# Kernel tuning notes

Hardware: AMD Instinct MI355X
Metric: run time of the kernel (lower is better)

## Reference

```python
import jax, jax.numpy as jnp
import numpy as np

IN_FEAT = 78
C = 128          # out_channels
H = 8            # nheads (layer 1)
B = 1024         # num graphs / batch
NPG = 32         # nodes per graph
N = B * NPG      # total nodes
EPG = 128        # edges per graph
E = B * EPG
GENE = 18000
PROT = 6688
FP = 2048        # drr/drc fingerprint size
N_TASKS = 1


def _lin(key, fan_in, fan_out):
    kw, kb = jax.random.split(key)
    s = 1.0 / np.sqrt(fan_in)
    W = jax.random.uniform(kw, (fan_in, fan_out), jnp.float32, -s, s)
    b = jax.random.uniform(kb, (fan_out,), jnp.float32, -s, s)
    return W, b


def setup_inputs() -> dict:
    key = jax.random.key(0)
    ks = jax.random.split(key, 32)
    goff = jnp.repeat(jnp.arange(B, dtype=jnp.int64) * NPG, EPG)
    e1s = jax.random.randint(ks[0], (E,), 0, NPG, dtype=jnp.int64) + goff
    e1d = jax.random.randint(ks[1], (E,), 0, NPG, dtype=jnp.int64) + goff
    e2s = jax.random.randint(ks[2], (E,), 0, NPG, dtype=jnp.int64) + goff
    e2d = jax.random.randint(ks[3], (E,), 0, NPG, dtype=jnp.int64) + goff
    inp = {
        "x1": jax.random.normal(ks[4], (N, IN_FEAT), jnp.float32),
        "x2": jax.random.normal(ks[5], (N, IN_FEAT), jnp.float32),
        "gene_exp": jax.random.uniform(ks[6], (B, GENE), jnp.float32),
        "drr": jax.random.uniform(ks[7], (B, FP), jnp.float32),
        "drc": jax.random.uniform(ks[8], (B, FP), jnp.float32),
        "prot_exp": jax.random.normal(ks[9], (B, PROT), jnp.float32),
        "edge_index1": jnp.stack([e1s, e1d]),
        "edge_index2": jnp.stack([e2s, e2d]),
        "batch": jnp.repeat(jnp.arange(B, dtype=jnp.int64), NPG),
    }
    W1, b1 = _lin(ks[10], IN_FEAT, H * C)
    inp.update(W_gat1=W1, b_gat1=b1,
               a_src1=jax.random.normal(ks[11], (H, C), jnp.float32) * 0.1,
               a_dst1=jax.random.normal(ks[12], (H, C), jnp.float32) * 0.1)
    # GAT layer 2: 1024 -> 128, 1 head
    W2, b2 = _lin(ks[13], H * C, C)
    inp.update(W_gat2=W2, b_gat2=b2,
               a_src2=jax.random.normal(ks[14], (1, C), jnp.float32) * 0.1,
               a_dst2=jax.random.normal(ks[15], (1, C), jnp.float32) * 0.1)
    inp["W_fcg"], inp["b_fcg"] = _lin(ks[16], C, C)
    # reduction MLP: gene -> 2048 -> 512 -> 2C
    inp["Wr1"], inp["br1"] = _lin(ks[17], GENE, 2048)
    inp["Wr2"], inp["br2"] = _lin(ks[18], 2048, 512)
    inp["Wr3"], inp["br3"] = _lin(ks[19], 512, 2 * C)
    # prot MLP: 6688 -> 1024 -> 512 -> 2C
    inp["Wp1"], inp["bp1"] = _lin(ks[20], PROT, 1024)
    inp["Wp2"], inp["bp2"] = _lin(ks[21], 1024, 512)
    inp["Wp3"], inp["bp3"] = _lin(ks[22], 512, 2 * C)
    # fingerprint fusion linears
    inp["Wdrr"], inp["bdrr"] = _lin(ks[23], C + FP, C + FP)
    inp["Wdrc"], inp["bdrc"] = _lin(ks[24], C + FP, C + FP)
    # predictor (3 layers): in = 2*(C+FP) + 2C + 2C = 4864 -> 512 -> 256 -> n_tasks
    in_dim = 2 * (C + FP) + 2 * C + 2 * C
    inp["Wf1"], inp["bf1"] = _lin(ks[25], in_dim, 512)
    inp["Wf2"], inp["bf2"] = _lin(ks[26], 512, 256)
    inp["Wout"], inp["bout"] = _lin(ks[27], 256, N_TASKS)
    return inp


def _gat(x, src, dst, W, a_src, a_dst, b, heads, ch):
    n = x.shape[0]
    # add self-loops (PyG GATConv default)
    sl = jnp.arange(n, dtype=src.dtype)
    src = jnp.concatenate([src, sl])
    dst = jnp.concatenate([dst, sl])
    h = (x @ W).reshape(n, heads, ch)                    # [N,H,C]
    a_s = (h * a_src).sum(-1)                            # [N,H]
    a_d = (h * a_dst).sum(-1)
    e = jax.nn.leaky_relu(a_s[src] + a_d[dst], 0.2)      # [E',H]
    m = jax.ops.segment_max(e, dst, num_segments=n)
    ex = jnp.exp(e - m[dst])
    den = jax.ops.segment_sum(ex, dst, num_segments=n)
    alpha = ex / (den[dst] + 1e-16)
    out = jax.ops.segment_sum(h[src] * alpha[:, :, None], dst, num_segments=n)
    return out.reshape(n, heads * ch) + b


def reference(x1, x2, gene_exp, drr, drc, prot_exp,
              W_gat1, b_gat1, a_src1, a_dst1,
              W_gat2, b_gat2, a_src2, a_dst2,
              W_fcg, b_fcg,
              Wr1, br1, Wr2, br2, Wr3, br3,
              Wp1, bp1, Wp2, bp2, Wp3, bp3,
              Wdrr, bdrr, Wdrc, bdrc,
              Wf1, bf1, Wf2, bf2, Wout, bout,
              edge_index1, edge_index2, batch):
    nb = gene_exp.shape[0]

    def drug_branch(x, ei):
        x = jax.nn.elu(_gat(x, ei[0], ei[1], W_gat1, a_src1, a_dst1, b_gat1, H, C))
        x = jax.nn.elu(_gat(x, ei[0], ei[1], W_gat2, a_src2, a_dst2, b_gat2, 1, C))
        x = jax.ops.segment_max(x, batch, num_segments=nb)   # global max pool
        return jax.nn.relu(x @ W_fcg + b_fcg)

    g1 = drug_branch(x1, edge_index1)
    g2 = drug_branch(x2, edge_index2)

    # gene branch: L2 row-normalize then MLP (dropout off at inference)
    norm = jnp.sqrt((gene_exp * gene_exp).sum(1, keepdims=True))
    cell = gene_exp / jnp.maximum(norm, 1e-12)
    cell = jax.nn.relu(cell @ Wr1 + br1)
    cell = jax.nn.relu(cell @ Wr2 + br2)
    cell_vec = jax.nn.relu(cell @ Wr3 + br3)

    # protein branch
    p = prot_exp.reshape(-1, PROT)
    p = jax.nn.elu(p @ Wp1 + bp1)
    p = jax.nn.elu(p @ Wp2 + bp2)
    p = jax.nn.relu(p @ Wp3 + bp3)

    # fingerprint fusion
    d1 = jnp.concatenate([g1, drr], axis=1)
    d2 = jnp.concatenate([g2, drc], axis=1)
    d1 = jax.nn.relu(d1 @ Wdrr + bdrr)
    d2 = jax.nn.relu(d2 @ Wdrc + bdrc)

    y = jnp.concatenate([d1, d2, cell_vec, p], axis=1)
    # 3-layer predictor
    y = jax.nn.relu(y @ Wf1 + bf1)
    y = jax.nn.relu(y @ Wf2 + bf2)
    out = y @ Wout + bout
    return out
```

## Files before the change

### kernel.cpp

```cpp
#include <hip/hip_runtime.h>
#include <math.h>

#define BATCH   1024
#define NPG     32
#define NNODES  (BATCH * NPG)
#define EPG     128
#define INFEAT  78
#define CCH     128
#define NHEAD   8
#define GENE    18000
#define GENEP   18016
#define PROT    6688
#define FPD     2048

#define ACT_NONE 0
#define ACT_RELU 1
#define ACT_ELU  2

typedef unsigned short ushort_t;
typedef __bf16 bf16x8_t __attribute__((ext_vector_type(8)));
typedef float  f32x4_t  __attribute__((ext_vector_type(4)));

__device__ __forceinline__ float b2f(ushort_t u) {
    return __uint_as_float(((unsigned)u) << 16);
}
__device__ __forceinline__ ushort_t f2b(float f) {
    unsigned x = __float_as_uint(f);
    return (ushort_t)((x + 0x7fffu + ((x >> 16) & 1u)) >> 16);
}

#define GBM 128
#define GBN 128
#define GBK 32

__device__ __forceinline__ void gemm_core(
    const ushort_t* __restrict__ A, const ushort_t* __restrict__ BT,
    int K, int kb, int ke, int row0, int col0,
    ushort_t* Asl, ushort_t* Bsl, f32x4_t acc[4][4])
{
    const int tid  = threadIdx.x;
    const int wave = tid >> 6;
    const int lane = tid & 63;
    const int wr   = wave >> 1;
    const int wc   = wave & 1;
    const int srow = lane >> 2;
    const int skel = (lane & 3) * 8;

    for (int k0 = kb; k0 < ke; k0 += GBK) {
        __syncthreads();
        #pragma unroll
        for (int t = 0; t < 2; ++t) {
            const int rg = wave * 32 + t * 16;
            const ushort_t* ga = A + (size_t)(row0 + rg + srow) * K + k0 + skel;
            __builtin_amdgcn_global_load_lds(
                (const __attribute__((address_space(1))) void*)ga,
                (__attribute__((address_space(3))) void*)&Asl[rg * GBK], 16, 0, 0);
            const ushort_t* gb = BT + (size_t)(col0 + rg + srow) * K + k0 + skel;
            __builtin_amdgcn_global_load_lds(
                (const __attribute__((address_space(1))) void*)gb,
                (__attribute__((address_space(3))) void*)&Bsl[rg * GBK], 16, 0, 0);
        }
        __syncthreads();

        const int fr = lane & 15;
        const int fq = lane >> 4;
        bf16x8_t av[4], bv[4];
        #pragma unroll
        for (int i = 0; i < 4; ++i)
            av[i] = *(const bf16x8_t*)&Asl[(wr * 64 + i * 16 + fr) * GBK + fq * 8];
        #pragma unroll
        for (int j = 0; j < 4; ++j)
            bv[j] = *(const bf16x8_t*)&Bsl[(wc * 64 + j * 16 + fr) * GBK + fq * 8];
        #pragma unroll
        for (int i = 0; i < 4; ++i)
            #pragma unroll
            for (int j = 0; j < 4; ++j)
                acc[i][j] = __builtin_amdgcn_mfma_f32_16x16x32_bf16(
                    av[i], bv[j], acc[i][j], 0, 0, 0);
    }
}

__global__ __launch_bounds__(256) void gemm_bf16_kernel(
    const ushort_t* __restrict__ A, const ushort_t* __restrict__ BT,
    const float* __restrict__ bias, ushort_t* __restrict__ C,
    int M, int N, int K, int act)
{
    __shared__ ushort_t Asl[GBM * GBK];
    __shared__ ushort_t Bsl[GBN * GBK];
    const int lane = threadIdx.x & 63;
    const int wave = threadIdx.x >> 6;
    const int wr = wave >> 1, wc = wave & 1;
    const int row0 = blockIdx.y * GBM;
    const int col0 = blockIdx.x * GBN;

    f32x4_t acc[4][4] = {};
    gemm_core(A, BT, K, 0, K, row0, col0, Asl, Bsl, acc);

    const int fr = lane & 15;
    const int fq = lane >> 4;
    #pragma unroll
    for (int i = 0; i < 4; ++i) {
        #pragma unroll
        for (int j = 0; j < 4; ++j) {
            const int gn = col0 + wc * 64 + j * 16 + fr;
            const float bb = bias ? bias[gn] : 0.0f;
            #pragma unroll
            for (int r = 0; r < 4; ++r) {
                const int gm = row0 + wr * 64 + i * 16 + fq * 4 + r;
                float v = acc[i][j][r] + bb;
                if (act == ACT_RELU)     v = fmaxf(v, 0.0f);
                else if (act == ACT_ELU) v = (v > 0.0f) ? v : (expf(v) - 1.0f);
                C[(size_t)gm * N + gn] = f2b(v);
            }
        }
    }
}

__global__ __launch_bounds__(256) void gemm_bf16_part_kernel(
    const ushort_t* __restrict__ A, const ushort_t* __restrict__ BT,
    float* __restrict__ part, int M, int N, int K, int KC)
{
    __shared__ ushort_t Asl[GBM * GBK];
    __shared__ ushort_t Bsl[GBN * GBK];
    const int lane = threadIdx.x & 63;
    const int wave = threadIdx.x >> 6;
    const int wr = wave >> 1, wc = wave & 1;
    const int row0 = blockIdx.y * GBM;
    const int col0 = blockIdx.x * GBN;
    const int z    = blockIdx.z;
    const int kb   = z * KC;
    const int ke   = min(K, kb + KC);

    f32x4_t acc[4][4] = {};
    gemm_core(A, BT, K, kb, ke, row0, col0, Asl, Bsl, acc);

    const int fr = lane & 15;
    const int fq = lane >> 4;
    float* po = part + (size_t)z * M * N;
    #pragma unroll
    for (int i = 0; i < 4; ++i)
        #pragma unroll
        for (int j = 0; j < 4; ++j) {
            const int gn = col0 + wc * 64 + j * 16 + fr;
            #pragma unroll
            for (int r = 0; r < 4; ++r) {
                const int gm = row0 + wr * 64 + i * 16 + fq * 4 + r;
                po[(size_t)gm * N + gn] = acc[i][j][r];
            }
        }
}

__global__ __launch_bounds__(256) void reduce_kernel(
    const float* __restrict__ part, const float* __restrict__ bias,
    ushort_t* __restrict__ C, int MN, int N, int S, int act)
{
    int i4 = (blockIdx.x * 256 + threadIdx.x) * 4;
    if (i4 >= MN) return;
    float4 s = *(const float4*)&part[i4];
    for (int z = 1; z < S; ++z) {
        float4 v = *(const float4*)&part[(size_t)z * MN + i4];
        s.x += v.x; s.y += v.y; s.z += v.z; s.w += v.w;
    }
    const int n = i4 % N;
    float o[4] = { s.x, s.y, s.z, s.w };
    if (bias) { o[0] += bias[n]; o[1] += bias[n+1]; o[2] += bias[n+2]; o[3] += bias[n+3]; }
    unsigned pk[2];
    ushort_t r[4];
    #pragma unroll
    for (int k = 0; k < 4; ++k) {
        float v = o[k];
        if (act == ACT_RELU)     v = fmaxf(v, 0.0f);
        else if (act == ACT_ELU) v = (v > 0.0f) ? v : (expf(v) - 1.0f);
        r[k] = f2b(v);
    }
    pk[0] = (unsigned)r[0] | ((unsigned)r[1] << 16);
    pk[1] = (unsigned)r[2] | ((unsigned)r[3] << 16);
    *(uint2*)&C[i4] = make_uint2(pk[0], pk[1]);
}

__global__ __launch_bounds__(256) void cast_rows_kernel(
    const float* __restrict__ src, const float* __restrict__ rowscale,
    ushort_t* __restrict__ dst, int R, int Cin, int Cpad)
{
    int idx = blockIdx.x * 256 + threadIdx.x;
    if (idx >= R * Cpad) return;
    int r = idx / Cpad, c = idx - r * Cpad;
    float v = 0.0f;
    if (c < Cin) {
        v = src[(size_t)r * Cin + c];
        if (rowscale) v *= rowscale[r];
    }
    dst[idx] = f2b(v);
}

__global__ __launch_bounds__(256) void castT_kernel(
    const float* __restrict__ W, ushort_t* __restrict__ WT,
    int K, int N, int Kpad)
{
    __shared__ float t[32][33];
    const int nb = blockIdx.x * 32, kb = blockIdx.y * 32;
    const int x = threadIdx.x & 31, y = threadIdx.x >> 5;
    #pragma unroll
    for (int yy = 0; yy < 32; yy += 8) {
        int k = kb + y + yy, n = nb + x;
        t[y + yy][x] = (k < K && n < N) ? W[(size_t)k * N + n] : 0.0f;
    }
    __syncthreads();
    #pragma unroll
    for (int yy = 0; yy < 32; yy += 8) {
        int n = nb + y + yy, kk = kb + x;
        if (n < N && kk < Kpad) WT[(size_t)n * Kpad + kk] = f2b(t[x][y + yy]);
    }
}

__device__ __forceinline__ unsigned enc_f(float f) {
    unsigned u = __float_as_uint(f);
    return (u >> 31) ? ~u : (u | 0x80000000u);
}
__device__ __forceinline__ float dec_f(unsigned e) {
    return (e >> 31) ? __uint_as_float(e ^ 0x80000000u) : __uint_as_float(~e);
}

template <int POOL>
__global__ __launch_bounds__(256) void gat_fused_kernel(
    const ushort_t* __restrict__ h, const int* __restrict__ esrc,
    const int* __restrict__ edst, const float* __restrict__ a_src,
    const float* __restrict__ a_dst, const float* __restrict__ bias,
    ushort_t* __restrict__ out, int H)
{
    const int g    = blockIdx.x / H;
    const int hd   = blockIdx.x % H;
    const int tid  = threadIdx.x;
    const int lane = tid & 63;
    const int wave = tid >> 6;
    const int base = g * NPG;
    const int HC   = H * CCH;

    __shared__ float h_l[NPG][CCH];
    __shared__ float At[NPG][NPG];
    __shared__ float asv[CCH], adv[CCH];
    __shared__ float as_l[NPG], ad_l[NPG];
    __shared__ unsigned m_l[NPG];
    __shared__ float den_l[NPG];
    __shared__ float sc_l[EPG + NPG];
    __shared__ unsigned char s_l[EPG + NPG], d_l[EPG + NPG];
    __shared__ float ptmp[2][CCH];

    {
        const int r4 = tid >> 6;
        const int cp = (tid & 63) * 2;
        #pragma unroll
        for (int rr = 0; rr < NPG; rr += 4) {
            const int r = rr + r4;
            unsigned v = *(const unsigned*)(h + (size_t)(base + r) * HC + hd * CCH + cp);
            h_l[r][cp]     = b2f((ushort_t)(v & 0xffff));
            h_l[r][cp + 1] = b2f((ushort_t)(v >> 16));
        }
    }
    #pragma unroll
    for (int i = tid; i < NPG * NPG; i += 256) ((float*)At)[i] = 0.0f;
    if (tid < CCH) asv[tid] = a_src[hd * CCH + tid];
    else           adv[tid - CCH] = a_dst[hd * CCH + tid - CCH];
    if (tid < NPG) { m_l[tid] = 0u; den_l[tid] = 0.0f; }
    __syncthreads();

    for (int n = wave; n < NPG; n += 4) {
        float v0 = h_l[n][lane], v1 = h_l[n][lane + 64];
        float s = v0 * asv[lane] + v1 * asv[lane + 64];
        float d = v0 * adv[lane] + v1 * adv[lane + 64];
        #pragma unroll
        for (int o = 32; o > 0; o >>= 1) {
            s += __shfl_xor(s, o, 64);
            d += __shfl_xor(d, o, 64);
        }
        if (lane == 0) { as_l[n] = s; ad_l[n] = d; }
    }
    __syncthreads();

    if (tid < EPG + NPG) {
        int s, d;
        if (tid < EPG) {
            s = esrc[g * EPG + tid] - base;
            d = edst[g * EPG + tid] - base;
        } else {
            s = d = tid - EPG;
        }
        float e = as_l[s] + ad_l[d];
        e = (e >= 0.0f) ? e : 0.2f * e;
        sc_l[tid] = e;
        s_l[tid] = (unsigned char)s;
        d_l[tid] = (unsigned char)d;
        atomicMax(&m_l[d], enc_f(e));
    }
    __syncthreads();

    if (tid < EPG + NPG) {
        float ex = expf(sc_l[tid] - dec_f(m_l[d_l[tid]]));
        sc_l[tid] = ex;
        atomicAdd(&den_l[d_l[tid]], ex);
    }
    __syncthreads();

    if (tid < EPG + NPG) {
        float al = sc_l[tid] / (den_l[d_l[tid]] + 1e-16f);
        atomicAdd(&At[s_l[tid]][d_l[tid]], al);
    }
    __syncthreads();

    const int c    = tid & 127;
    const int half = tid >> 7;
    float acc[16] = {};
    #pragma unroll 4
    for (int s = 0; s < NPG; ++s) {
        const float hv = h_l[s][c];
        const float4* ap = (const float4*)&At[s][half * 16];
        #pragma unroll
        for (int q = 0; q < 4; ++q) {
            float4 av = ap[q];
            acc[q * 4 + 0] += av.x * hv;
            acc[q * 4 + 1] += av.y * hv;
            acc[q * 4 + 2] += av.z * hv;
            acc[q * 4 + 3] += av.w * hv;
        }
    }

    const float bb = bias[hd * CCH + c];
    if (POOL) {
        float m = -INFINITY;
        #pragma unroll
        for (int r = 0; r < 16; ++r) {
            float v = acc[r] + bb;
            v = (v > 0.0f) ? v : (expf(v) - 1.0f);
            m = fmaxf(m, v);
        }
        ptmp[half][c] = m;
        __syncthreads();
        if (tid < CCH)
            out[(size_t)g * CCH + tid] = f2b(fmaxf(ptmp[0][tid], ptmp[1][tid]));
    } else {
        #pragma unroll
        for (int r = 0; r < 16; ++r) {
            float v = acc[r] + bb;
            v = (v > 0.0f) ? v : (expf(v) - 1.0f);
            out[(size_t)(base + half * 16 + r) * HC + hd * CCH + c] = f2b(v);
        }
    }
}

__global__ __launch_bounds__(256) void rownorm_kernel(
    const float* __restrict__ x, float* __restrict__ inv, int K)
{
    const int row = blockIdx.x;
    const int tid = threadIdx.x;
    const float* xp = x + (size_t)row * K;
    float s = 0.f;
    for (int k = tid; k < K; k += 256) { float v = xp[k]; s += v * v; }
    __shared__ float red[256];
    red[tid] = s;
    __syncthreads();
    for (int o = 128; o > 0; o >>= 1) {
        if (tid < o) red[tid] += red[tid + o];
        __syncthreads();
    }
    if (tid == 0) inv[row] = 1.0f / fmaxf(sqrtf(red[0]), 1e-12f);
}

__global__ __launch_bounds__(256) void copyb_kernel(
    ushort_t* __restrict__ dst, int ld, int off,
    const ushort_t* __restrict__ src, int rows, int cols)
{
    int idx = blockIdx.x * 256 + threadIdx.x;
    if (idx >= rows * cols) return;
    int r = idx / cols, c = idx - r * cols;
    dst[(size_t)r * ld + off + c] = src[idx];
}

__global__ __launch_bounds__(256) void castcols_kernel(
    ushort_t* __restrict__ dst, int ld, int off,
    const float* __restrict__ src, int rows, int cols)
{
    int idx = blockIdx.x * 256 + threadIdx.x;
    if (idx >= rows * cols) return;
    int r = idx / cols, c = idx - r * cols;
    dst[(size_t)r * ld + off + c] = f2b(src[idx]);
}

__global__ __launch_bounds__(256) void final_kernel(
    const ushort_t* __restrict__ y, const float* __restrict__ w,
    const float* __restrict__ b, float* __restrict__ out)
{
    const int row = blockIdx.x;
    const int tid = threadIdx.x;
    float v = b2f(y[(size_t)row * 256 + tid]) * w[tid];
    __shared__ float red[256];
    red[tid] = v;
    __syncthreads();
    for (int o = 128; o > 0; o >>= 1) {
        if (tid < o) red[tid] += red[tid + o];
        __syncthreads();
    }
    if (tid == 0) out[row] = red[0] + b[0];
}

static inline void launch_gemm(const ushort_t* A, const ushort_t* BT,
                               const float* bias, ushort_t* C,
                               int M, int N, int K, int act, hipStream_t stream)
{
    dim3 grid(N / GBN, M / GBM);
    gemm_bf16_kernel<<<grid, 256, 0, stream>>>(A, BT, bias, C, M, N, K, act);
}

static inline void launch_gemm_sk(const ushort_t* A, const ushort_t* BT,
                                  const float* bias, ushort_t* C, float* part,
                                  int M, int N, int K, int S, int act,
                                  hipStream_t stream)
{
    if (S <= 1) { launch_gemm(A, BT, bias, C, M, N, K, act, stream); return; }
    const int iters = K / GBK;
    const int ipc   = (iters + S - 1) / S;
    const int S_eff = (iters + ipc - 1) / ipc;
    const int KC    = ipc * GBK;
    dim3 grid(N / GBN, M / GBM, S_eff);
    gemm_bf16_part_kernel<<<grid, 256, 0, stream>>>(A, BT, part, M, N, K, KC);
    const int MN = M * N;
    reduce_kernel<<<(MN / 4 + 255) / 256, 256, 0, stream>>>(
        part, bias, C, MN, N, S_eff, act);
}

static inline void launch_castT(const float* W, ushort_t* WT, int K, int N,
                                int Kpad, hipStream_t stream)
{
    dim3 grid((N + 31) / 32, (Kpad + 31) / 32);
    castT_kernel<<<grid, 256, 0, stream>>>(W, WT, K, N, Kpad);
}

extern "C" void kernel_launch(void* const* d_in, const int* in_sizes, int n_in,
                              void* d_out, int out_size, void* d_ws, size_t ws_size,
                              hipStream_t stream)
{
    const float* x1      = (const float*)d_in[0];
    const float* x2      = (const float*)d_in[1];
    const float* gene    = (const float*)d_in[2];
    const float* drr     = (const float*)d_in[3];
    const float* drc     = (const float*)d_in[4];
    const float* prot    = (const float*)d_in[5];
    const int*   ei1     = (const int*)d_in[6];
    const int*   ei2     = (const int*)d_in[7];
    const float* W_gat1  = (const float*)d_in[9];
    const float* b_gat1  = (const float*)d_in[10];
    const float* a_src1  = (const float*)d_in[11];
    const float* a_dst1  = (const float*)d_in[12];
    const float* W_gat2  = (const float*)d_in[13];
    const float* b_gat2  = (const float*)d_in[14];
    const float* a_src2  = (const float*)d_in[15];
    const float* a_dst2  = (const float*)d_in[16];
    const float* W_fcg   = (const float*)d_in[17];
    const float* b_fcg   = (const float*)d_in[18];
    const float* Wr1     = (const float*)d_in[19];
    const float* br1     = (const float*)d_in[20];
    const float* Wr2     = (const float*)d_in[21];
    const float* br2     = (const float*)d_in[22];
    const float* Wr3     = (const float*)d_in[23];
    const float* br3     = (const float*)d_in[24];
    const float* Wp1     = (const float*)d_in[25];
    const float* bp1     = (const float*)d_in[26];
    const float* Wp2     = (const float*)d_in[27];
    const float* bp2     = (const float*)d_in[28];
    const float* Wp3     = (const float*)d_in[29];
    const float* bp3     = (const float*)d_in[30];
    const float* Wdrr    = (const float*)d_in[31];
    const float* bdrr    = (const float*)d_in[32];
    const float* Wdrc    = (const float*)d_in[33];
    const float* bdrc    = (const float*)d_in[34];
    const float* Wf1     = (const float*)d_in[35];
    const float* bf1     = (const float*)d_in[36];
    const float* Wf2     = (const float*)d_in[37];
    const float* bf2     = (const float*)d_in[38];
    const float* Wout    = (const float*)d_in[39];
    const float* bout    = (const float*)d_in[40];
    float* outp = (float*)d_out;

    char* ws = (char*)d_ws;
    size_t off = 0;
    auto alloc = [&](size_t bytes) -> char* {
        char* r = ws + off;
        off += (bytes + 255) & ~(size_t)255;
        return r;
    };

    char* BIG0 = alloc(134217728);
    char* BIG1 = alloc(67108864);

    ushort_t* go1f   = (ushort_t*)BIG0;
    ushort_t* h1     = (ushort_t*)BIG1;
    float*    part   = (float*)BIG1;
    ushort_t* WT_r1  = (ushort_t*)(BIG0 + 0);
    ushort_t* gene_nb= (ushort_t*)(BIG0 + 73793536);
    ushort_t* cell1  = (ushort_t*)(BIG0 + 110690304);
    ushort_t* WT_r2  = (ushort_t*)(BIG0 + 114884608);
    ushort_t* WT_p2  = (ushort_t*)(BIG0 + 116981760);
    ushort_t* WT_p1  = (ushort_t*)(BIG0 + 118030336);

    ushort_t* xb     = (ushort_t*)alloc((size_t)NNODES * 96 * 2);
    char*     h2reg  = alloc((size_t)2 * NNODES * 128 * 2);
    char*     catreg = alloc((size_t)2 * 1024 * 2176 * 2);
    ushort_t* h2f    = (ushort_t*)h2reg;
    ushort_t* protb  = (ushort_t*)h2reg;
    ushort_t* cat1   = (ushort_t*)catreg;
    ushort_t* cat2   = (ushort_t*)(catreg + (size_t)1024 * 2176 * 2);
    ushort_t* pooled = (ushort_t*)alloc((size_t)2 * BATCH * 128 * 2);
    ushort_t* gpair  = (ushort_t*)alloc((size_t)2 * BATCH * 128 * 2);
    float*    invn   = (float*)alloc((size_t)BATCH * 4);
    ushort_t* cvec   = (ushort_t*)alloc((size_t)BATCH * 256 * 2);
    ushort_t* pvec   = (ushort_t*)alloc((size_t)BATCH * 256 * 2);
    ushort_t* y1     = (ushort_t*)alloc((size_t)BATCH * 512 * 2);
    ushort_t* y2     = (ushort_t*)alloc((size_t)BATCH * 256 * 2);
    ushort_t* WT_g1  = (ushort_t*)alloc((size_t)1024 * 96 * 2);
    ushort_t* WT_g2  = (ushort_t*)alloc((size_t)128 * 1024 * 2);
    ushort_t* WT_fcg = (ushort_t*)alloc((size_t)128 * 128 * 2);
    ushort_t* WT_r3  = (ushort_t*)alloc((size_t)256 * 512 * 2);
    ushort_t* WT_p3  = (ushort_t*)alloc((size_t)256 * 512 * 2);
    ushort_t* WT_f2  = (ushort_t*)alloc((size_t)256 * 512 * 2);
    ushort_t* WT_drr = (ushort_t*)alloc((size_t)2176 * 2176 * 2);
    ushort_t* WT_drc = (ushort_t*)alloc((size_t)2176 * 2176 * 2);
    ushort_t* WT_f1  = (ushort_t*)alloc((size_t)512 * 4864 * 2);
    ushort_t* p1b    = (ushort_t*)alloc((size_t)1024 * 1024 * 2);
    ushort_t* p2b    = (ushort_t*)alloc((size_t)1024 * 512 * 2);
    ushort_t* cell2  = (ushort_t*)alloc((size_t)1024 * 512 * 2);
    ushort_t* d1     = (ushort_t*)alloc((size_t)1024 * 2176 * 2);
    ushort_t* d2     = (ushort_t*)alloc((size_t)1024 * 2176 * 2);
    ushort_t* ybuf   = (ushort_t*)alloc((size_t)1024 * 4864 * 2);

    const int E = in_sizes[6] / 2;

    launch_castT(W_gat1, WT_g1, INFEAT, 1024, 96, stream);
    launch_castT(W_gat2, WT_g2, 1024, 128, 1024, stream);
    launch_castT(W_fcg,  WT_fcg, 128, 128, 128, stream);

    for (int drug = 0; drug < 2; drug++) {
        const float* x  = drug ? x2 : x1;
        const int*   es = (drug ? ei2 : ei1);
        const int*   ed = es + E;
        ushort_t* go1d = go1f + (size_t)drug * NNODES * 1024;

        cast_rows_kernel<<<(NNODES * 96 + 255) / 256, 256, 0, stream>>>(
            x, nullptr, xb, NNODES, INFEAT, 96);
        launch_gemm(xb, WT_g1, nullptr, h1, NNODES, 1024, 96, ACT_NONE, stream);
        gat_fused_kernel<0><<<BATCH * NHEAD, 256, 0, stream>>>(
            h1, es, ed, a_src1, a_dst1, b_gat1, go1d, NHEAD);
    }

    launch_gemm(go1f, WT_g2, nullptr, h2f, 2 * NNODES, 128, 1024, ACT_NONE, stream);

    launch_castT(Wr1, WT_r1, GENE, 2048, GENEP, stream);
    launch_castT(Wr2, WT_r2, 2048, 512, 2048, stream);
    launch_castT(Wp1, WT_p1, PROT, 1024, PROT, stream);
    launch_castT(Wp2, WT_p2, 1024, 512, 1024, stream);
    launch_castT(Wr3, WT_r3, 512, 256, 512, stream);
    launch_castT(Wp3, WT_p3, 512, 256, 512, stream);
    launch_castT(Wf2, WT_f2, 512, 256, 512, stream);
    launch_castT(Wdrr, WT_drr, 2176, 2176, 2176, stream);
    launch_castT(Wdrc, WT_drc, 2176, 2176, 2176, stream);
    launch_castT(Wf1, WT_f1, 4864, 512, 4864, stream);

    for (int drug = 0; drug < 2; drug++) {
        const int* es = (drug ? ei2 : ei1);
        const int* ed = es + E;
        gat_fused_kernel<1><<<BATCH, 256, 0, stream>>>(
            h2f + (size_t)drug * NNODES * 128, es, ed,
            a_src2, a_dst2, b_gat2, pooled + (size_t)drug * BATCH * 128, 1);
    }
    launch_gemm(pooled, WT_fcg, b_fcg, gpair, 2 * BATCH, 128, 128, ACT_RELU, stream);

    rownorm_kernel<<<BATCH, 256, 0, stream>>>(gene, invn, GENE);
    cast_rows_kernel<<<(BATCH * GENEP + 255) / 256, 256, 0, stream>>>(
        gene, invn, gene_nb, BATCH, GENE, GENEP);
    launch_gemm_sk(gene_nb, WT_r1, br1, cell1, part, BATCH, 2048, GENEP, 8, ACT_RELU, stream);
    launch_gemm_sk(cell1, WT_r2, br2, cell2, part, BATCH, 512, 2048, 8, ACT_RELU, stream);
    launch_gemm_sk(cell2, WT_r3, br3, cvec, part, BATCH, 256, 512, 4, ACT_RELU, stream);

    cast_rows_kernel<<<(BATCH * PROT + 255) / 256, 256, 0, stream>>>(
        prot, nullptr, protb, BATCH, PROT, PROT);
    launch_gemm_sk(protb, WT_p1, bp1, p1b, part, BATCH, 1024, PROT, 8, ACT_ELU, stream);
    launch_gemm_sk(p1b, WT_p2, bp2, p2b, part, BATCH, 512, 1024, 4, ACT_ELU, stream);
    launch_gemm_sk(p2b, WT_p3, bp3, pvec, part, BATCH, 256, 512, 4, ACT_RELU, stream);

    {
        int n = BATCH * CCH;
        copyb_kernel<<<(n + 255) / 256, 256, 0, stream>>>(cat1, 2176, 0, gpair, BATCH, CCH);
        copyb_kernel<<<(n + 255) / 256, 256, 0, stream>>>(cat2, 2176, 0, gpair + BATCH * CCH, BATCH, CCH);
        n = BATCH * FPD;
        castcols_kernel<<<(n + 255) / 256, 256, 0, stream>>>(cat1, 2176, CCH, drr, BATCH, FPD);
        castcols_kernel<<<(n + 255) / 256, 256, 0, stream>>>(cat2, 2176, CCH, drc, BATCH, FPD);
    }
    launch_gemm_sk(cat1, WT_drr, bdrr, d1, part, BATCH, 2176, 2176, 4, ACT_RELU, stream);
    launch_gemm_sk(cat2, WT_drc, bdrc, d2, part, BATCH, 2176, 2176, 4, ACT_RELU, stream);

    {
        int n = BATCH * 2176;
        copyb_kernel<<<(n + 255) / 256, 256, 0, stream>>>(ybuf, 4864, 0,    d1, BATCH, 2176);
        copyb_kernel<<<(n + 255) / 256, 256, 0, stream>>>(ybuf, 4864, 2176, d2, BATCH, 2176);
        n = BATCH * 256;
        copyb_kernel<<<(n + 255) / 256, 256, 0, stream>>>(ybuf, 4864, 4352, cvec, BATCH, 256);
        copyb_kernel<<<(n + 255) / 256, 256, 0, stream>>>(ybuf, 4864, 4608, pvec, BATCH, 256);
    }
    launch_gemm_sk(ybuf, WT_f1, bf1, y1, part, BATCH, 512, 4864, 8, ACT_RELU, stream);
    launch_gemm_sk(y1, WT_f2, bf2, y2, part, BATCH, 256, 512, 4, ACT_RELU, stream);
    final_kernel<<<BATCH, 256, 0, stream>>>(y2, Wout, bout, outp);
}
```

Before: 1.256 ms.

## Add 256x256 eight-phase pipelined split-K GEMM for gene and protein layers

Adds a new 512-thread bf16 MFMA GEMM kernel with 256x256 tiles, 128KB double-buffered LDS filled by direct global-to-LDS loads, XOR swizzling, an XCD-aware workgroup remap, and eight interleaved phases of LDS reads, staging and MFMA with setprio. It is used for the two large-K first layers (gene 18000 and protein 6688), with K padded to multiples of 128 and the workspace offsets moved to fit. The aim is to raise MFMA utilisation and hide memory latency on these bandwidth-heavy GEMMs. The cost is more complex synchronisation, larger padded casts, and a partial-sum reduction that still runs afterwards.

New measurement: 1.188 ms. 5.4% less time.

```diff
diff --git a/kernel.cpp b/kernel.cpp
--- a/kernel.cpp
+++ b/kernel.cpp
@@ -9,8 +9,9 @@
 #define CCH     128
 #define NHEAD   8
 #define GENE    18000
-#define GENEP   18016
+#define GENEP   18048
 #define PROT    6688
+#define PROTP   6784
 #define FPD     2048
 
 #define ACT_NONE 0
@@ -178,6 +179,172 @@
     *(uint2*)&C[i4] = make_uint2(pk[0], pk[1]);
 }
 
+#define DSREAD(dst, addr) asm volatile("ds_read_b128 %0, %1" : "=v"(dst) : "v"(addr))
+
+template <int MH>
+__device__ __forceinline__ void read_A8(bf16x8_t (&av)[4][2], unsigned b0, unsigned b1)
+{
+    DSREAD(av[0][0], b0 + (MH * 4 + 0) * 2048);
+    DSREAD(av[0][1], b1 + (MH * 4 + 0) * 2048);
+    DSREAD(av[1][0], b0 + (MH * 4 + 1) * 2048);
+    DSREAD(av[1][1], b1 + (MH * 4 + 1) * 2048);
+    DSREAD(av[2][0], b0 + (MH * 4 + 2) * 2048);
+    DSREAD(av[2][1], b1 + (MH * 4 + 2) * 2048);
+    DSREAD(av[3][0], b0 + (MH * 4 + 3) * 2048);
+    DSREAD(av[3][1], b1 + (MH * 4 + 3) * 2048);
+}
+
+template <int NH>
+__device__ __forceinline__ void read_B8(bf16x8_t (&bvh)[2][2], unsigned b0, unsigned b1)
+{
+    DSREAD(bvh[0][0], b0 + (NH * 2 + 0) * 2048);
+    DSREAD(bvh[0][1], b1 + (NH * 2 + 0) * 2048);
+    DSREAD(bvh[1][0], b0 + (NH * 2 + 1) * 2048);
+    DSREAD(bvh[1][1], b1 + (NH * 2 + 1) * 2048);
+}
+
+template <int MH, int NH>
+__device__ __forceinline__ void mfma_quad(const bf16x8_t (&av)[4][2],
+                                          const bf16x8_t (&bvh)[2][2],
+                                          f32x4_t (&acc)[8][4])
+{
+    #pragma unroll
+    for (int qq = 0; qq < 4; ++qq)
+        #pragma unroll
+        for (int pp = 0; pp < 2; ++pp)
+            #pragma unroll
+            for (int ss = 0; ss < 2; ++ss)
+                acc[MH * 4 + qq][NH * 2 + pp] = __builtin_amdgcn_mfma_f32_16x16x32_bf16(
+                    av[qq][ss], bvh[pp][ss], acc[MH * 4 + qq][NH * 2 + pp], 0, 0, 0);
+}
+
+__device__ __forceinline__ void stage_half8(
+    const ushort_t* __restrict__ G, int rc0, int K, int kt,
+    unsigned lo0, ushort_t* smemp, int tid)
+{
+    const int lane = tid & 63;
+    const int ce = (((lane & 7) ^ ((lane >> 3) & 7)) << 3);
+    #pragma unroll
+    for (int j = 0; j < 2; ++j) {
+        const int rr = j * 64 + (tid >> 3);
+        const ushort_t* g = G + (size_t)(rc0 + rr) * K + kt + ce;
+        const unsigned lo = lo0 + (unsigned)((j * 64 + ((tid >> 3) & ~7)) * 128);
+        __builtin_amdgcn_global_load_lds(
+            (const __attribute__((address_space(1))) void*)g,
+            (__attribute__((address_space(3))) void*)((char*)smemp + lo),
+            16, 0, 0);
+    }
+}
+
+#define PH_TAIL(MH, NH, BVH, VM) \
+    __builtin_amdgcn_s_barrier(); \
+    asm volatile("s_waitcnt lgkmcnt(0)"); \
+    __builtin_amdgcn_sched_barrier(0); \
+    __builtin_amdgcn_s_setprio(1); \
+    mfma_quad<MH, NH>(av, BVH, acc); \
+    __builtin_amdgcn_s_setprio(0); \
+    __builtin_amdgcn_sched_barrier(0); \
+    if (VM) asm volatile("s_waitcnt vmcnt(4)"); \
+    __builtin_amdgcn_s_barrier();
+
+__global__ __launch_bounds__(512, 2) void gemm_bf16_8ph_kernel(
+    const ushort_t* __restrict__ A, const ushort_t* __restrict__ BT,
+    float* __restrict__ part, int M, int N, int K, int IPC)
+{
+    extern __shared__ ushort_t smem8[];
+    const int tid  = threadIdx.x;
+    const int lane = tid & 63;
+    const int wid  = tid >> 6;
+    const int wm = wid >> 2, wn = wid & 3;
+    const int fr = lane & 15, fq = lane >> 4;
+
+    const int gx = N >> 8, gy = M >> 8;
+    const int nwg = (int)gridDim.x;
+    const int q8 = nwg >> 3, r8 = nwg & 7;
+    const int xcd = (int)blockIdx.x & 7, sub = (int)blockIdx.x >> 3;
+    const int wg = (xcd < r8 ? xcd * (q8 + 1) : r8 * (q8 + 1) + (xcd - r8) * q8) + sub;
+    const int bz  = wg / (gx * gy);
+    const int rem = wg - bz * gx * gy;
+    const int by  = rem / gx;
+    const int bx  = rem - by * gx;
+    const int row0 = by << 8, col0 = bx << 8;
+
+    const int iters = K >> 7;
+    const int k0    = bz * IPC * 128;
+    const int nit   = min(IPC, iters - bz * IPC);
+
+    const unsigned SB  = (unsigned)(size_t)(__attribute__((address_space(3))) void*)smem8;
+    const unsigned xa  = (unsigned)((fr & 7) << 4);
+    const unsigned cs0 = ((unsigned)(fq * 16)) ^ xa;
+    const unsigned cs1 = ((unsigned)(64 + fq * 16)) ^ xa;
+    const unsigned arow = SB + (unsigned)((wm * 128 + fr) * 128);
+    const unsigned brow = SB + 32768u + (unsigned)((wn * 64 + fr) * 128);
+
+    f32x4_t  acc[8][4] = {};
+    bf16x8_t av[4][2];
+    bf16x8_t bv[2][2][2];
+
+    auto KT = [&](int tt) { int kt = k0 + tt * 64; return kt > K - 64 ? K - 64 : kt; };
+    auto STA = [&](int tt, int h) {
+        stage_half8(A, row0 + h * 128, K, KT(tt),
+                    (unsigned)(((tt & 1) * 65536) + h * 16384), smem8, tid);
+    };
+    auto STB = [&](int tt, int h) {
+        stage_half8(BT, col0 + h * 128, K, KT(tt),
+                    (unsigned)(((tt & 1) * 65536) + 32768 + h * 16384), smem8, tid);
+    };
+
+    STB(0, 0); STB(0, 1); STA(0, 0); STA(0, 1); STB(1, 0); STB(1, 1);
+    asm volatile("s_waitcnt vmcnt(4)");
+    __builtin_amdgcn_s_barrier();
+
+    for (int it = 0; it < nit; ++it) {
+        const int t = it << 1;
+        read_A8<0>(av, arow + cs0, arow + cs1);
+        read_B8<0>(bv[0], brow + cs0, brow + cs1);
+        STA(t + 1, 0);
+        PH_TAIL(0, 0, bv[0], 0)
+
+        read_B8<1>(bv[1], brow + cs0, brow + cs1);
+        STA(t + 1, 1);
+        PH_TAIL(0, 1, bv[1], 0)
+
+        read_A8<1>(av, arow + cs0, arow + cs1);
+        STB(t + 2, 0);
+        PH_TAIL(1, 0, bv[0], 0)
+
+        STB(t + 2, 1);
+        PH_TAIL(1, 1, bv[1], 1)
+
+        read_A8<0>(av, arow + 65536u + cs0, arow + 65536u + cs1);
+        read_B8<0>(bv[0], brow + 65536u + cs0, brow + 65536u + cs1);
+        STA(t + 2, 0);
+        PH_TAIL(0, 0, bv[0], 0)
+
+        read_B8<1>(bv[1], brow + 65536u + cs0, brow + 65536u + cs1);
+        STA(t + 2, 1);
+        PH_TAIL(0, 1, bv[1], 0)
+
+        read_A8<1>(av, arow + 65536u + cs0, arow + 65536u + cs1);
+        STB(t + 3, 0);
+        PH_TAIL(1, 0, bv[0], 0)
+
+        STB(t + 3, 1);
+        PH_TAIL(1, 1, bv[1], 1)
+    }
+
+    float* po = part + (size_t)bz * M * N;
+    const int gmb = row0 + wm * 128 + fq * 4;
+    const int gnb = col0 + wn * 64 + fr;
+    #pragma unroll
+    for (int mi = 0; mi < 8; ++mi)
+        #pragma unroll
+        for (int nj = 0; nj < 4; ++nj)
+            #pragma unroll
+            for (int r2 = 0; r2 < 4; ++r2)
+                po[(size_t)(gmb + mi * 16 + r2) * N + (gnb + nj * 16)] = acc[mi][nj][r2];
+}
+
 __global__ __launch_bounds__(256) void cast_rows_kernel(
     const float* __restrict__ src, const float* __restrict__ rowscale,
     ushort_t* __restrict__ dst, int R, int Cin, int Cpad)
@@ -422,6 +589,28 @@
     const int KC    = ipc * GBK;
     dim3 grid(N / GBN, M / GBM, S_eff);
     gemm_bf16_part_kernel<<<grid, 256, 0, stream>>>(A, BT, part, M, N, K, KC);
+    const int MN = M * N;
+    reduce_kernel<<<(MN / 4 + 255) / 256, 256, 0, stream>>>(
+        part, bias, C, MN, N, S_eff, act);
+}
+
+static inline void launch_gemm_8ph(const ushort_t* A, const ushort_t* BT,
+                                   const float* bias, ushort_t* C, float* part,
+                                   int M, int N, int K, int S, int act,
+                                   hipStream_t stream)
+{
+    const int iters = K >> 7;
+    const int ipc   = (iters + S - 1) / S;
+    const int S_eff = (iters + ipc - 1) / ipc;
+    const int gx = N >> 8, gy = M >> 8;
+    const int nwg = gx * gy * S_eff;
+    static bool attr_done = false;
+    if (!attr_done) {
+        (void)hipFuncSetAttribute((const void*)gemm_bf16_8ph_kernel,
+                                  hipFuncAttributeMaxDynamicSharedMemorySize, 131072);
+        attr_done = true;
+    }
+    gemm_bf16_8ph_kernel<<<dim3(nwg), 512, 131072, stream>>>(A, BT, part, M, N, K, ipc);
     const int MN = M * N;
     reduce_kernel<<<(MN / 4 + 255) / 256, 256, 0, stream>>>(
         part, bias, C, MN, N, S_eff, act);
@@ -495,11 +684,11 @@
     ushort_t* h1     = (ushort_t*)BIG1;
     float*    part   = (float*)BIG1;
     ushort_t* WT_r1  = (ushort_t*)(BIG0 + 0);
-    ushort_t* gene_nb= (ushort_t*)(BIG0 + 73793536);
-    ushort_t* cell1  = (ushort_t*)(BIG0 + 110690304);
-    ushort_t* WT_r2  = (ushort_t*)(BIG0 + 114884608);
-    ushort_t* WT_p2  = (ushort_t*)(BIG0 + 116981760);
-    ushort_t* WT_p1  = (ushort_t*)(BIG0 + 118030336);
+    ushort_t* gene_nb= (ushort_t*)(BIG0 + 73924608);
+    ushort_t* cell1  = (ushort_t*)(BIG0 + 110886912);
+    ushort_t* WT_r2  = (ushort_t*)(BIG0 + 115081216);
+    ushort_t* WT_p2  = (ushort_t*)(BIG0 + 117178368);
+    ushort_t* WT_p1  = (ushort_t*)(BIG0 + 118226944);
 
     ushort_t* xb     = (ushort_t*)alloc((size_t)NNODES * 96 * 2);
     char*     h2reg  = alloc((size_t)2 * NNODES * 128 * 2);
@@ -554,7 +743,7 @@
 
     launch_castT(Wr1, WT_r1, GENE, 2048, GENEP, stream);
     launch_castT(Wr2, WT_r2, 2048, 512, 2048, stream);
-    launch_castT(Wp1, WT_p1, PROT, 1024, PROT, stream);
+    launch_castT(Wp1, WT_p1, PROT, 1024, PROTP, stream);
     launch_castT(Wp2, WT_p2, 1024, 512, 1024, stream);
     launch_castT(Wr3, WT_r3, 512, 256, 512, stream);
     launch_castT(Wp3, WT_p3, 512, 256, 512, stream);
@@ -575,13 +764,13 @@
     rownorm_kernel<<<BATCH, 256, 0, stream>>>(gene, invn, GENE);
     cast_rows_kernel<<<(BATCH * GENEP + 255) / 256, 256, 0, stream>>>(
         gene, invn, gene_nb, BATCH, GENE, GENEP);
-    launch_gemm_sk(gene_nb, WT_r1, br1, cell1, part, BATCH, 2048, GENEP, 8, ACT_RELU, stream);
+    launch_gemm_8ph(gene_nb, WT_r1, br1, cell1, part, BATCH, 2048, GENEP, 8, ACT_RELU, stream);
     launch_gemm_sk(cell1, WT_r2, br2, cell2, part, BATCH, 512, 2048, 8, ACT_RELU, stream);
     launch_gemm_sk(cell2, WT_r3, br3, cvec, part, BATCH, 256, 512, 4, ACT_RELU, stream);
 
-    cast_rows_kernel<<<(BATCH * PROT + 255) / 256, 256, 0, stream>>>(
-        prot, nullptr, protb, BATCH, PROT, PROT);
-    launch_gemm_sk(protb, WT_p1, bp1, p1b, part, BATCH, 1024, PROT, 8, ACT_ELU, stream);
+    cast_rows_kernel<<<(BATCH * PROTP + 255) / 256, 256, 0, stream>>>(
+        prot, nullptr, protb, BATCH, PROT, PROTP);
+    launch_gemm_8ph(protb, WT_p1, bp1, p1b, part, BATCH, 1024, PROTP, 16, ACT_ELU, stream);
     launch_gemm_sk(p1b, WT_p2, bp2, p2b, part, BATCH, 512, 1024, 4, ACT_ELU, stream);
     launch_gemm_sk(p2b, WT_p3, bp3, pvec, part, BATCH, 256, 512, 4, ACT_RELU, stream);
 
```
